# Performance work log

Measured on AMD Instinct MI355X. Metric: run time of the kernel, lower is better.

The kernel has to match this reference:

```python
import jax, jax.numpy as jnp
import numpy as np

T = 2048          # tokens (single causal sequence)
HID = 4096        # hidden_size
H = 32            # num_heads
DQ = 256          # per-head q/k dim (192 nope + 64 rope)
DN = 192          # nope dim
DR = 64           # rope dim
DV = 256          # v head dim
DKV = 512         # kv latent rank
QLORA = 2048      # q lora rank
EPS = 1e-6
THETA = 10000.0
SCALE = DQ ** -0.5


def rmsnorm(x, w):
    return x * jax.lax.rsqrt(jnp.mean(x * x, axis=-1, keepdims=True) + EPS) * w


def rope_neox(pos, x):
    # x: [T, h, DR]; neox style: rotate concatenated halves
    inv_freq = 1.0 / (THETA ** (jnp.arange(0, DR, 2, dtype=jnp.float32) / DR))  # [DR/2]
    ang = pos.astype(jnp.float32)[:, None] * inv_freq  # [T, DR/2]
    cos = jnp.cos(ang)[:, None, :]
    sin = jnp.sin(ang)[:, None, :]
    x1, x2 = jnp.split(x, 2, axis=-1)
    return jnp.concatenate([x1 * cos - x2 * sin, x2 * cos + x1 * sin], axis=-1)


def setup_inputs() -> dict:
    key = jax.random.key(0)
    ks = jax.random.split(key, 8)
    s = 0.02
    return {
        "hidden_states": jax.random.normal(ks[0], (T, HID), dtype=jnp.float32),
        "positions": jnp.arange(T, dtype=jnp.int32),
        "wq_a": jax.random.normal(ks[1], (HID, QLORA), dtype=jnp.float32) * s,
        "q_a_ln_w": jnp.ones((QLORA,), dtype=jnp.float32),
        "wq_b": jax.random.normal(ks[2], (QLORA, H * DQ), dtype=jnp.float32) * s,
        "wkv_a": jax.random.normal(ks[3], (HID, DKV + DR), dtype=jnp.float32) * s,
        "kv_a_ln_w": jnp.ones((DKV,), dtype=jnp.float32),
        "wkv_b": jax.random.normal(ks[4], (DKV, H * (DN + DV)), dtype=jnp.float32) * s,
        "wo": jax.random.normal(ks[5], (H * DV, HID), dtype=jnp.float32) * s,
    }


def reference(hidden_states, positions, wq_a, q_a_ln_w, wq_b, wkv_a, kv_a_ln_w, wkv_b, wo):
    # q path: lora down -> rmsnorm -> up -> [T, H, 256]
    q = rmsnorm(hidden_states @ wq_a, q_a_ln_w)
    q = (q @ wq_b).reshape(T, H, DQ)
    # kv path: latent 512 + shared k_pe 64
    latent = hidden_states @ wkv_a
    kv_a, k_pe = jnp.split(latent, [DKV], axis=-1)
    kv_a = rmsnorm(kv_a, kv_a_ln_w)
    kv = (kv_a @ wkv_b).reshape(T, H, DN + DV)
    k_nope, v = jnp.split(kv, [DN], axis=-1)
    q_nope, q_pe = jnp.split(q, [DN], axis=-1)
    k_pe = k_pe.reshape(T, 1, DR)
    q_pe = rope_neox(positions, q_pe)
    k_pe = rope_neox(positions, k_pe)
    q = jnp.concatenate([q_nope, q_pe], axis=-1)                       # [T, H, 256]
    k = jnp.concatenate([k_nope, jnp.broadcast_to(k_pe, (T, H, DR))], axis=-1)
    # causal attention
    scores = jnp.einsum("thd,shd->hts", q, k) * SCALE                  # [H, T, T]
    causal = jnp.tril(jnp.ones((T, T), dtype=bool))
    scores = jnp.where(causal[None], scores, jnp.finfo(scores.dtype).min)
    attn = jax.nn.softmax(scores, axis=-1)
    out = jnp.einsum("hts,shd->thd", attn, v).reshape(T, H * DV)
    return out @ wo
```

## Files before the change

kernel.cpp:

```cpp
#include <hip/hip_runtime.h>
#include <cstdint>
#include <cstddef>

#define T_    2048
#define HID_  4096
#define NH_   32
#define DQ_   256
#define DN_   192
#define DR_   64
#define DV_   256
#define DKV_  512
#define QL_   2048
#define NKV_  576
#define HDQ_  8192
#define HDKV_ 14336
#define HDV_  8192
#define SCALE_ 0.0625f
#define MN5_  8388608
#define SK5_  2
#define NKC_  2816
#define PS1_  5767168
#define SK1_  4

using bf16x8 = __attribute__((ext_vector_type(8))) short;
using f32x4  = __attribute__((ext_vector_type(4))) float;

__device__ ushort g_hb   [(size_t)T_*HID_];
__device__ ushort g_wtc  [(size_t)NKC_*HID_];
__device__ ushort g_wtqb [(size_t)HDQ_*QL_];
__device__ ushort g_wtkvb[(size_t)HDKV_*DKV_];
__device__ ushort g_wto  [(size_t)HID_*HDV_];
__device__ float  g_qa   [(size_t)T_*QL_];
__device__ ushort g_qn   [(size_t)T_*QL_];
__device__ ushort g_q    [(size_t)T_*HDQ_];
__device__ ushort g_kvn  [(size_t)T_*DKV_];
__device__ ushort g_kv   [(size_t)T_*HDKV_];
__device__ ushort g_k    [(size_t)NH_*T_*DQ_];
__device__ ushort g_vt   [(size_t)NH_*DV_*T_];
__device__ ushort g_o    [(size_t)T_*HDV_];
__device__ float  g_p5   [(size_t)SK1_*PS1_];

__device__ __forceinline__ float b2f(ushort h){ union{unsigned u; float f;} x; x.u=((unsigned)h)<<16; return x.f; }
__device__ __forceinline__ ushort f2b(float f){ union{float f; unsigned u;} x; x.f=f; unsigned r=x.u + 0x7fffu + ((x.u>>16)&1u); return (ushort)(r>>16); }
__device__ __forceinline__ void storeC(float*  p, float v){ *p = v; }
__device__ __forceinline__ void storeC(ushort* p, float v){ *p = f2b(v); }

#define GLD16(gp, lp) __builtin_amdgcn_global_load_lds( \
    (const __attribute__((address_space(1))) unsigned*)(gp), \
    (__attribute__((address_space(3))) unsigned*)(lp), 16, 0, 0)

__global__ __launch_bounds__(256) void convert_hidden(const float* __restrict__ src) {
  size_t i = ((size_t)blockIdx.x*256 + threadIdx.x)*4;
  float4 v = *(const float4*)(src + i);
  ushort4 o; o.x=f2b(v.x); o.y=f2b(v.y); o.z=f2b(v.z); o.w=f2b(v.w);
  *(ushort4*)(g_hb + i) = o;
}

__global__ __launch_bounds__(256) void transpose_all(const float* __restrict__ wqa,
                                                     const float* __restrict__ wkva,
                                                     const float* __restrict__ wqb,
                                                     const float* __restrict__ wkvb,
                                                     const float* __restrict__ wo) {
  int bid = blockIdx.x;
  const float* W; ushort* Wt; int K, N, gx;
  if (bid < 4096)       { W=wqa;  Wt=g_wtc;                      K=HID_; N=QL_;   gx=64; }
  else if (bid < 5632)  { W=wkva; Wt=g_wtc+(size_t)QL_*HID_;     K=HID_; N=NKV_;  gx=64;  bid-=4096; }
  else if (bid < 13824) { W=wqb;  Wt=g_wtqb;                     K=QL_;  N=HDQ_;  gx=32;  bid-=5632; }
  else if (bid < 17408) { W=wkvb; Wt=g_wtkvb;                    K=DKV_; N=HDKV_; gx=8;   bid-=13824; }
  else                  { W=wo;   Wt=g_wto;                      K=HDV_; N=HID_;  gx=128; bid-=17408; }
  const int bk = (bid % gx)*64, bn = (bid / gx)*32;

  __shared__ float tile[64][33];
  const int tx = threadIdx.x & 31, ty = threadIdx.x >> 5;
  for (int r = ty; r < 64; r += 8) {
    int n = bn + tx;
    tile[r][tx] = (n < N) ? W[(size_t)(bk + r)*N + n] : 0.f;
  }
  __syncthreads();
  for (int rr = ty; rr < 32; rr += 8) {
    int n = bn + rr;
    unsigned pv = (unsigned)f2b(tile[2*tx][rr]) | ((unsigned)f2b(tile[2*tx+1][rr]) << 16);
    ((unsigned*)(Wt + (size_t)n*K))[(bk>>1) + tx] = pv;
  }
}

template<typename OutT, int S, int EPI>
__device__ __forceinline__ void gemm8_body(ushort* sm,
                                           const ushort* __restrict__ A,
                                           const ushort* __restrict__ Bt,
                                           OutT* __restrict__ C,
                                           int M, int N, int Kfull, int pstride,
                                           int id, int nb) {
  const int tid = threadIdx.x, lane = tid & 63, w = tid >> 6;
  const int wr = w >> 2, wc = w & 3, l15 = lane & 15, l4 = lane >> 4;
  const int swm = (l15 & 7) << 3;
  const int gm = M >> 8, gn = N >> 8;
  const int swz = (id & 7) * (nb >> 3) + (id >> 3);
  const int m0 = (swz % gm) << 8;
  const int rest = swz / gm;
  const int n0 = (rest % gn) << 8;
  const int ks = rest / gn;
  const int Ksl = Kfull / S;
  const int kofs = ks * Ksl;
  const int NT = Ksl >> 6;

#define STG_A(tt, qm) do { const int p_=(tt)&1, kb_=kofs+(tt)*64; \
    _Pragma("unroll") \
    for (int i_=0;i_<2;i_++){ \
      const int le_=(i_*512+tid)*8, r_=le_>>6, c_=le_&63; \
      const int tr_=(r_>>6)*128 + (qm)*64 + (r_&63); \
      GLD16(A + (size_t)(m0+tr_)*Kfull + kb_ + (c_ ^ ((r_&7)<<3)), \
            sm + p_*16384 + (qm)*8192 + le_); } } while(0)
#define STG_B(tt, qn) do { const int p_=(tt)&1, kb_=kofs+(tt)*64; \
    _Pragma("unroll") \
    for (int i_=0;i_<2;i_++){ \
      const int le_=(i_*512+tid)*8, r_=le_>>6, c_=le_&63; \
      const int tr_=(r_>>5)*64 + (qn)*32 + (r_&31); \
      GLD16(Bt + (size_t)(n0+tr_)*Kfull + kb_ + (c_ ^ ((r_&7)<<3)), \
            sm + 32768 + p_*16384 + (qn)*8192 + le_); } } while(0)

  f32x4 acc[8][4];
  #pragma unroll
  for (int i=0;i<8;i++)
    #pragma unroll
    for (int j=0;j<4;j++) acc[i][j] = f32x4{0.f,0.f,0.f,0.f};

  STG_A(0,0); STG_B(0,0); STG_A(0,1); STG_B(0,1);
  if (NT > 1) { STG_A(1,0); STG_B(1,0); }
  __builtin_amdgcn_sched_barrier(0);
  if (NT > 1) asm volatile("s_waitcnt vmcnt(4)" ::: "memory");
  else        asm volatile("s_waitcnt vmcnt(0)" ::: "memory");
  __builtin_amdgcn_sched_barrier(0);
  __builtin_amdgcn_s_barrier();

  for (int t = 0; t < NT; ++t) {
    const int p = t & 1;
    const ushort* Ab = sm + p*16384;
    const ushort* Bb = sm + 32768 + p*16384;
    bf16x8 af[4][2], bq0[2][2], bq1[2][2];

    #pragma unroll
    for (int mi=0;mi<4;mi++)
      #pragma unroll
      for (int k2=0;k2<2;k2++)
        af[mi][k2] = *(const bf16x8*)(Ab + (wr*64 + mi*16 + l15)*64 + ((k2*32 + 8*l4) ^ swm));
    #pragma unroll
    for (int nf=0;nf<2;nf++)
      #pragma unroll
      for (int k2=0;k2<2;k2++)
        bq0[nf][k2] = *(const bf16x8*)(Bb + (wc*32 + nf*16 + l15)*64 + ((k2*32 + 8*l4) ^ swm));
    if (t + 1 < NT) STG_A(t+1, 1);
    __builtin_amdgcn_sched_barrier(0);
    __builtin_amdgcn_s_barrier();
    __builtin_amdgcn_s_setprio(1);
    #pragma unroll
    for (int mi=0;mi<4;mi++)
      #pragma unroll
      for (int nf=0;nf<2;nf++)
        #pragma unroll
        for (int k2=0;k2<2;k2++)
          acc[mi][nf] = __builtin_amdgcn_mfma_f32_16x16x32_bf16(af[mi][k2], bq0[nf][k2], acc[mi][nf], 0,0,0);
    __builtin_amdgcn_s_setprio(0);
    __builtin_amdgcn_sched_barrier(0);
    __builtin_amdgcn_s_barrier();

    #pragma unroll
    for (int nf=0;nf<2;nf++)
      #pragma unroll
      for (int k2=0;k2<2;k2++)
        bq1[nf][k2] = *(const bf16x8*)(Bb + 8192 + (wc*32 + nf*16 + l15)*64 + ((k2*32 + 8*l4) ^ swm));
    if (t + 1 < NT) STG_B(t+1, 1);
    __builtin_amdgcn_sched_barrier(0);
    __builtin_amdgcn_s_barrier();
    __builtin_amdgcn_s_setprio(1);
    #pragma unroll
    for (int mi=0;mi<4;mi++)
      #pragma unroll
      for (int nf=0;nf<2;nf++)
        #pragma unroll
        for (int k2=0;k2<2;k2++)
          acc[mi][2+nf] = __builtin_amdgcn_mfma_f32_16x16x32_bf16(af[mi][k2], bq1[nf][k2], acc[mi][2+nf], 0,0,0);
    __builtin_amdgcn_s_setprio(0);
    __builtin_amdgcn_sched_barrier(0);
    __builtin_amdgcn_s_barrier();

    #pragma unroll
    for (int mi=0;mi<4;mi++)
      #pragma unroll
      for (int k2=0;k2<2;k2++)
        af[mi][k2] = *(const bf16x8*)(Ab + 8192 + (wr*64 + mi*16 + l15)*64 + ((k2*32 + 8*l4) ^ swm));
    if (t + 2 < NT) STG_A(t+2, 0);
    __builtin_amdgcn_sched_barrier(0);
    __builtin_amdgcn_s_barrier();
    __builtin_amdgcn_s_setprio(1);
    #pragma unroll
    for (int mi=0;mi<4;mi++)
      #pragma unroll
      for (int nf=0;nf<2;nf++)
        #pragma unroll
        for (int k2=0;k2<2;k2++)
          acc[4+mi][nf] = __builtin_amdgcn_mfma_f32_16x16x32_bf16(af[mi][k2], bq0[nf][k2], acc[4+mi][nf], 0,0,0);
    __builtin_amdgcn_s_setprio(0);
    __builtin_amdgcn_sched_barrier(0);
    __builtin_amdgcn_s_barrier();

    if (t + 2 < NT) STG_B(t+2, 0);
    __builtin_amdgcn_sched_barrier(0);
    if (t + 2 < NT)      asm volatile("s_waitcnt vmcnt(4)" ::: "memory");
    else if (t + 1 < NT) asm volatile("s_waitcnt vmcnt(0)" ::: "memory");
    __builtin_amdgcn_sched_barrier(0);
    __builtin_amdgcn_s_barrier();
    __builtin_amdgcn_s_setprio(1);
    #pragma unroll
    for (int mi=0;mi<4;mi++)
      #pragma unroll
      for (int nf=0;nf<2;nf++)
        #pragma unroll
        for (int k2=0;k2<2;k2++)
          acc[4+mi][2+nf] = __builtin_amdgcn_mfma_f32_16x16x32_bf16(af[mi][k2], bq1[nf][k2], acc[4+mi][2+nf], 0,0,0);
    __builtin_amdgcn_s_setprio(0);
    __builtin_amdgcn_sched_barrier(0);
    __builtin_amdgcn_s_barrier();
  }
#undef STG_A
#undef STG_B
  asm volatile("s_waitcnt vmcnt(0)" ::: "memory");

  #pragma unroll
  for (int mi=0;mi<8;mi++)
    #pragma unroll
    for (int nj=0;nj<4;nj++) {
      const int row = m0 + wr*128 + mi*16 + l4*4;
      const int col = n0 + wc*64 + nj*16 + l15;
      if (EPI == 2) {
        const int h = col / 448, j = col - h*448;
        #pragma unroll
        for (int r=0;r<4;r++) {
          ushort v = f2b(acc[mi][nj][r]);
          if (j < DN_) g_k[((size_t)h*T_ + row + r)*DQ_ + j] = v;
          else         g_kv[(size_t)(row + r)*HDKV_ + col]   = v;
        }
      } else {
        #pragma unroll
        for (int r=0;r<4;r++) {
          if (S == 1) storeC(&C[(size_t)(row+r)*N + col], acc[mi][nj][r]);
          else ((float*)C)[(size_t)ks*pstride + (size_t)(row+r)*N + col] = acc[mi][nj][r];
        }
      }
    }
}

template<typename OutT, int S, int EPI>
__global__ __launch_bounds__(512, 2) void gemm8(const ushort* __restrict__ A,
                                                const ushort* __restrict__ Bt,
                                                OutT* __restrict__ C,
                                                int M, int N, int Kfull, int pstride) {
  __shared__ ushort sm[65536];
  gemm8_body<OutT,S,EPI>(sm, A, Bt, C, M, N, Kfull, pstride, blockIdx.x, gridDim.x);
}

__global__ __launch_bounds__(512, 2) void gemm_up_dual(const ushort* __restrict__ qn,
                                                       const ushort* __restrict__ wtqb,
                                                       ushort* __restrict__ q,
                                                       const ushort* __restrict__ kvn,
                                                       const ushort* __restrict__ wtkvb) {
  __shared__ ushort sm[65536];
  if (blockIdx.x < 256)
    gemm8_body<ushort,1,0>(sm, qn, wtqb, q, T_, HDQ_, QL_, 0, blockIdx.x, 256);
  else
    gemm8_body<ushort,1,2>(sm, kvn, wtkvb, (ushort*)nullptr, T_, HDKV_, DKV_, 0, blockIdx.x - 256, 448);
}

__global__ __launch_bounds__(256) void reduce5(const float* __restrict__ p, float* __restrict__ out) {
  size_t i = ((size_t)blockIdx.x*256 + threadIdx.x)*4;
  float4 a = *(const float4*)(p + i);
  #pragma unroll
  for (int s=1; s<SK5_; s++) {
    float4 b = *(const float4*)(p + (size_t)s*MN5_ + i);
    a.x+=b.x; a.y+=b.y; a.z+=b.z; a.w+=b.w;
  }
  *(float4*)(out + i) = a;
}

__global__ __launch_bounds__(256) void rmsnorm_q(const float* __restrict__ p,
                                                 const float* __restrict__ wln) {
  const int row = blockIdx.x;
  const float* x = p + (size_t)row*NKC_;
  float* xo = g_qa + (size_t)row*QL_;
  float ss = 0.f;
  for (int i = threadIdx.x; i < QL_/4; i += 256) {
    float4 v = *(const float4*)(x + i*4);
    #pragma unroll
    for (int s=1; s<SK1_; s++) {
      float4 b = *(const float4*)(x + (size_t)s*PS1_ + i*4);
      v.x+=b.x; v.y+=b.y; v.z+=b.z; v.w+=b.w;
    }
    ((float4*)xo)[i] = v;
    ss += v.x*v.x + v.y*v.y + v.z*v.z + v.w*v.w;
  }
  #pragma unroll
  for (int o=32;o>=1;o>>=1) ss += __shfl_xor(ss, o);
  __shared__ float sr[4];
  if ((threadIdx.x & 63) == 0) sr[threadIdx.x>>6] = ss;
  __syncthreads();
  float rs = rsqrtf((sr[0]+sr[1]+sr[2]+sr[3])/(float)QL_ + 1e-6f);
  for (int i = threadIdx.x; i < QL_; i += 256)
    g_qn[(size_t)row*QL_ + i] = f2b(xo[i]*rs*wln[i]);
}

__global__ __launch_bounds__(256) void kv_norm_rope(const float* __restrict__ p,
                                                    const float* __restrict__ wln,
                                                    const int* __restrict__ pos) {
  const int t = blockIdx.x;
  const float* base = p + (size_t)t*NKC_ + QL_;
  __shared__ float lat[NKV_];
  float ss = 0.f;
  for (int i = threadIdx.x; i < NKV_; i += 256) {
    float v = base[i];
    #pragma unroll
    for (int s=1; s<SK1_; s++) v += base[(size_t)s*PS1_ + i];
    lat[i] = v;
    if (i < DKV_) ss += v*v;
  }
  #pragma unroll
  for (int o=32;o>=1;o>>=1) ss += __shfl_xor(ss, o);
  __shared__ float sr[4];
  if ((threadIdx.x & 63) == 0) sr[threadIdx.x>>6] = ss;
  __syncthreads();
  float rs = rsqrtf((sr[0]+sr[1]+sr[2]+sr[3])/(float)DKV_ + 1e-6f);
  for (int i = threadIdx.x; i < DKV_; i += 256)
    g_kvn[(size_t)t*DKV_ + i] = f2b(lat[i]*rs*wln[i]);
  {
    const int i = threadIdx.x & 31, hb = threadIdx.x >> 5;
    float pp = (float)pos[t];
    float ang = pp * powf(10000.f, -(float)i/32.f);
    float c = cosf(ang), s = sinf(ang);
    float x1 = lat[DKV_ + i], x2 = lat[DKV_ + 32 + i];
    ushort k1 = f2b(x1*c - x2*s);
    ushort k2 = f2b(x2*c + x1*s);
    #pragma unroll
    for (int hh = 0; hh < 4; ++hh) {
      const int h = hb + hh*8;
      g_k[((size_t)h*T_ + t)*DQ_ + DN_ + i]      = k1;
      g_k[((size_t)h*T_ + t)*DQ_ + DN_ + 32 + i] = k2;
    }
  }
}

__global__ __launch_bounds__(256) void q_rope(const int* __restrict__ pos) {
  const int t = blockIdx.x;
  __shared__ float cs[32], sn[32];
  if (threadIdx.x < 32) {
    const int i = threadIdx.x;
    float p = (float)pos[t];
    float ang = p * powf(10000.f, -(float)i/32.f);
    cs[i] = cosf(ang); sn[i] = sinf(ang);
  }
  __syncthreads();
  for (int e = threadIdx.x; e < NH_*32; e += 256) {
    const int h = e >> 5, i = e & 31;
    ushort* qp = g_q + (size_t)t*HDQ_ + h*DQ_ + DN_;
    float x1 = b2f(qp[i]), x2 = b2f(qp[32 + i]);
    qp[i]      = f2b(x1*cs[i] - x2*sn[i]);
    qp[32 + i] = f2b(x2*cs[i] + x1*sn[i]);
  }
}

__global__ __launch_bounds__(256) void build_vt() {
  const int h = blockIdx.x, tt = blockIdx.y;
  __shared__ ushort tile[64*272];
  const int tid = threadIdx.x;
  #pragma unroll
  for (int p=0;p<8;p++) {
    int le = (p*256+tid)*8;
    int tl = le >> 8, d = le & 255;
    uint4 v = *(const uint4*)(g_kv + (size_t)(tt*64 + tl)*HDKV_ + h*448 + DN_ + d);
    *(uint4*)(tile + tl*272 + d) = v;
  }
  __syncthreads();
  #pragma unroll
  for (int p=0;p<8;p++) {
    int le = (p*256+tid)*8;
    int d = le >> 6, tl0 = le & 63;
    ushort tmp[8];
    #pragma unroll
    for (int j=0;j<8;j++) tmp[j] = tile[(tl0+j)*272 + d];
    *(uint4*)(g_vt + ((size_t)h*DV_ + d)*T_ + tt*64 + tl0) = *(const uint4*)tmp;
  }
}

__global__ __launch_bounds__(256) void attn_kernel() {
  __shared__ ushort KV[64*256];
  __shared__ ushort Pl[4][16][64];
  const int h = blockIdx.x;
  const int qt = (gridDim.y - 1) - blockIdx.y;
  const int tid = threadIdx.x, lane = tid & 63, w = tid >> 6;
  const int l15 = lane & 15, l4 = lane >> 4;
  const int swm = (l15 & 7) << 3;

  const ushort* Kh = g_k  + (size_t)h*T_*DQ_;
  const ushort* Vh = g_vt + (size_t)h*DV_*T_;

#define STAGE_K(kt_) do { \
    const ushort* ks_ = Kh + (size_t)(kt_)*64*DQ_; \
    _Pragma("unroll") \
    for (int c_=0;c_<8;c_++){ int le_=(c_*256+tid)*8, r_=le_>>8, co_=le_&255; \
      GLD16(ks_ + r_*256 + (co_ ^ ((r_&7)<<3)), KV+le_); } } while(0)
#define STAGE_V(kt_) do { \
    _Pragma("unroll") \
    for (int c_=0;c_<8;c_++){ int le_=(c_*256+tid)*8, d_=le_>>6, kv_=le_&63; \
      GLD16(Vh + (size_t)d_*T_ + (kt_)*64 + (kv_ ^ ((d_&7)<<3)), KV+le_); } } while(0)

  const int q0 = qt*64;
  const int qrow = q0 + w*16 + l15;

  bf16x8 qf[8];
  {
    const ushort* qb = g_q + (size_t)qrow*HDQ_ + h*DQ_;
    #pragma unroll
    for (int g=0; g<8; g++) qf[g] = *(const bf16x8*)(qb + 32*g + 8*l4);
  }
  f32x4 acc[16];
  #pragma unroll
  for (int i=0;i<16;i++) acc[i] = f32x4{0.f,0.f,0.f,0.f};
  float m_r = -1e30f, l_r = 0.f;

  STAGE_K(0);

  for (int kt = 0; kt <= qt; ++kt) {
    __builtin_amdgcn_sched_barrier(0);
    asm volatile("s_waitcnt vmcnt(0)" ::: "memory");
    __builtin_amdgcn_sched_barrier(0);
    __builtin_amdgcn_s_barrier();

    f32x4 s[4];
    #pragma unroll
    for (int fn=0; fn<4; fn++) s[fn] = f32x4{0.f,0.f,0.f,0.f};
    __builtin_amdgcn_s_setprio(1);
    #pragma unroll
    for (int g=0; g<8; g++)
      #pragma unroll
      for (int fn=0; fn<4; fn++) {
        bf16x8 kf = *(const bf16x8*)(KV + (fn*16 + l15)*256 + ((32*g + 8*l4) ^ swm));
        s[fn] = __builtin_amdgcn_mfma_f32_16x16x32_bf16(kf, qf[g], s[fn], 0,0,0);
      }
    __builtin_amdgcn_s_setprio(0);
    asm volatile("s_waitcnt lgkmcnt(0)" ::: "memory");
    __builtin_amdgcn_sched_barrier(0);
    __builtin_amdgcn_s_barrier();
    STAGE_V(kt);
    __builtin_amdgcn_sched_barrier(0);

    if (kt == qt) {
      #pragma unroll
      for (int fn=0; fn<4; fn++)
        #pragma unroll
        for (int r=0;r<4;r++) {
          int kv = kt*64 + fn*16 + l4*4 + r;
          if (kv > qrow) s[fn][r] = -1e30f;
        }
    }

    float mx = s[0][0];
    #pragma unroll
    for (int fn=0; fn<4; fn++)
      #pragma unroll
      for (int r=0;r<4;r++) mx = fmaxf(mx, s[fn][r]);
    mx = fmaxf(mx, __shfl_xor(mx, 16));
    mx = fmaxf(mx, __shfl_xor(mx, 32));
    mx *= SCALE_;
    if (__any(mx > m_r)) {
      float mn = fmaxf(m_r, mx);
      float sc = __expf(m_r - mn);
      m_r = mn;
      l_r *= sc;
      #pragma unroll
      for (int fd=0; fd<16; fd++)
        #pragma unroll
        for (int r=0;r<4;r++) acc[fd][r] *= sc;
    }
    float ssum = 0.f;
    #pragma unroll
    for (int fn=0; fn<4; fn++)
      #pragma unroll
      for (int r=0;r<4;r++) {
        float p = __expf(fmaf(s[fn][r], SCALE_, -m_r));
        s[fn][r] = p; ssum += p;
      }
    ssum += __shfl_xor(ssum, 16);
    ssum += __shfl_xor(ssum, 32);
    l_r += ssum;

    #pragma unroll
    for (int fn=0; fn<4; fn++) {
      ushort4 pw;
      pw.x = f2b(s[fn][0]); pw.y = f2b(s[fn][1]);
      pw.z = f2b(s[fn][2]); pw.w = f2b(s[fn][3]);
      *(ushort4*)(&Pl[w][l15][(fn*16 + l4*4) ^ swm]) = pw;
    }

    __builtin_amdgcn_sched_barrier(0);
    asm volatile("s_waitcnt vmcnt(0)" ::: "memory");
    __builtin_amdgcn_sched_barrier(0);
    __builtin_amdgcn_s_barrier();

    __builtin_amdgcn_s_setprio(1);
    #pragma unroll
    for (int s2=0; s2<2; s2++) {
      bf16x8 pa = *(const bf16x8*)(&Pl[w][l15][(s2*32 + 8*l4) ^ swm]);
      #pragma unroll
      for (int fd=0; fd<16; fd++) {
        bf16x8 vb = *(const bf16x8*)(KV + (fd*16 + l15)*64 + ((s2*32 + 8*l4) ^ swm));
        acc[fd] = __builtin_amdgcn_mfma_f32_16x16x32_bf16(vb, pa, acc[fd], 0,0,0);
      }
    }
    __builtin_amdgcn_s_setprio(0);
    asm volatile("s_waitcnt lgkmcnt(0)" ::: "memory");
    __builtin_amdgcn_sched_barrier(0);
    __builtin_amdgcn_s_barrier();
    if (kt < qt) STAGE_K(kt+1);
    __builtin_amdgcn_sched_barrier(0);
  }

  l_r = 1.f / l_r;
  #pragma unroll
  for (int fd=0; fd<16; fd++) {
    ushort4 ow;
    ow.x = f2b(acc[fd][0] * l_r); ow.y = f2b(acc[fd][1] * l_r);
    ow.z = f2b(acc[fd][2] * l_r); ow.w = f2b(acc[fd][3] * l_r);
    *(ushort4*)(g_o + (size_t)qrow*HDV_ + h*DV_ + fd*16 + l4*4) = ow;
  }
#undef STAGE_K
#undef STAGE_V
}

extern "C" void kernel_launch(void* const* d_in, const int* in_sizes, int n_in,
                              void* d_out, int out_size, void* d_ws, size_t ws_size,
                              hipStream_t stream) {
  (void)in_sizes; (void)n_in; (void)d_ws; (void)ws_size; (void)out_size;
  const float* hs    = (const float*)d_in[0];
  const int*   pos   = (const int*)  d_in[1];
  const float* wqa   = (const float*)d_in[2];
  const float* qlnw  = (const float*)d_in[3];
  const float* wqb   = (const float*)d_in[4];
  const float* wkva  = (const float*)d_in[5];
  const float* kvlnw = (const float*)d_in[6];
  const float* wkvb  = (const float*)d_in[7];
  const float* wo    = (const float*)d_in[8];
  float* out = (float*)d_out;

  void *p_hb, *p_wtc, *p_wtqb, *p_wtkvb, *p_wto;
  void *p_qn, *p_q, *p_kvn, *p_kv, *p_o, *p_p5;
  hipGetSymbolAddress(&p_hb,    HIP_SYMBOL(g_hb));
  hipGetSymbolAddress(&p_wtc,   HIP_SYMBOL(g_wtc));
  hipGetSymbolAddress(&p_wtqb,  HIP_SYMBOL(g_wtqb));
  hipGetSymbolAddress(&p_wtkvb, HIP_SYMBOL(g_wtkvb));
  hipGetSymbolAddress(&p_wto,   HIP_SYMBOL(g_wto));
  hipGetSymbolAddress(&p_qn,    HIP_SYMBOL(g_qn));
  hipGetSymbolAddress(&p_q,     HIP_SYMBOL(g_q));
  hipGetSymbolAddress(&p_kvn,   HIP_SYMBOL(g_kvn));
  hipGetSymbolAddress(&p_kv,    HIP_SYMBOL(g_kv));
  hipGetSymbolAddress(&p_o,     HIP_SYMBOL(g_o));
  hipGetSymbolAddress(&p_p5,    HIP_SYMBOL(g_p5));

  convert_hidden<<<8192, 256, 0, stream>>>(hs);
  transpose_all<<<33792, 256, 0, stream>>>(wqa, wkva, wqb, wkvb, wo);

  gemm8<float,SK1_,1><<<(T_/256)*(NKC_/256)*SK1_, 512, 0, stream>>>((const ushort*)p_hb, (const ushort*)p_wtc, (float*)p_p5, T_, NKC_, HID_, PS1_);
  rmsnorm_q<<<T_, 256, 0, stream>>>((const float*)p_p5, qlnw);
  kv_norm_rope<<<T_, 256, 0, stream>>>((const float*)p_p5, kvlnw, pos);

  gemm_up_dual<<<704, 512, 0, stream>>>((const ushort*)p_qn, (const ushort*)p_wtqb, (ushort*)p_q,
                                        (const ushort*)p_kvn, (const ushort*)p_wtkvb);
  q_rope<<<T_, 256, 0, stream>>>(pos);

  build_vt<<<dim3(NH_, T_/64), 256, 0, stream>>>();
  attn_kernel<<<dim3(NH_, 32), 256, 0, stream>>>();

  gemm8<float,SK5_,1><<<(T_/256)*(HID_/256)*SK5_, 512, 0, stream>>>((const ushort*)p_o, (const ushort*)p_wto, (float*)p_p5, T_, HID_, HDV_, MN5_);
  reduce5<<<MN5_/1024, 256, 0, stream>>>((const float*)p_p5, out);
}
```

Before: 747.1 us.

## Split K/V LDS buffers in attention and fold hidden conversion into transpose

The attention kernel now gives K and V^T their own shared-memory buffers, so both tiles are loaded together at the end of each iteration. This removes the mid-iteration wait and barrier pairs that existed only because the two tiles shared one buffer. The price is more LDS per block (about 72KB), which can lower how many blocks fit on a CU. Separately, the hidden-state fp32-to-bf16 conversion is folded into the weight transpose launch as extra blocks, saving one kernel launch.

Measured after the change: 759.8 us. Within noise of the previous version (+1.7%).

```diff
diff --git a/kernel.cpp b/kernel.cpp
--- a/kernel.cpp
+++ b/kernel.cpp
@@ -49,19 +49,21 @@
     (const __attribute__((address_space(1))) unsigned*)(gp), \
     (__attribute__((address_space(3))) unsigned*)(lp), 16, 0, 0)
 
-__global__ __launch_bounds__(256) void convert_hidden(const float* __restrict__ src) {
-  size_t i = ((size_t)blockIdx.x*256 + threadIdx.x)*4;
-  float4 v = *(const float4*)(src + i);
-  ushort4 o; o.x=f2b(v.x); o.y=f2b(v.y); o.z=f2b(v.z); o.w=f2b(v.w);
-  *(ushort4*)(g_hb + i) = o;
-}
-
-__global__ __launch_bounds__(256) void transpose_all(const float* __restrict__ wqa,
+__global__ __launch_bounds__(256) void transpose_all(const float* __restrict__ hs,
+                                                     const float* __restrict__ wqa,
                                                      const float* __restrict__ wkva,
                                                      const float* __restrict__ wqb,
                                                      const float* __restrict__ wkvb,
                                                      const float* __restrict__ wo) {
   int bid = blockIdx.x;
+  if (bid < 8192) {
+    size_t i = ((size_t)bid*256 + threadIdx.x)*4;
+    float4 v = *(const float4*)(hs + i);
+    ushort4 o; o.x=f2b(v.x); o.y=f2b(v.y); o.z=f2b(v.z); o.w=f2b(v.w);
+    *(ushort4*)(g_hb + i) = o;
+    return;
+  }
+  bid -= 8192;
   const float* W; ushort* Wt; int K, N, gx;
   if (bid < 4096)       { W=wqa;  Wt=g_wtc;                      K=HID_; N=QL_;   gx=64; }
   else if (bid < 5632)  { W=wkva; Wt=g_wtc+(size_t)QL_*HID_;     K=HID_; N=NKV_;  gx=64;  bid-=4096; }
@@ -390,7 +392,8 @@
 }
 
 __global__ __launch_bounds__(256) void attn_kernel() {
-  __shared__ ushort KV[64*256];
+  __shared__ ushort Ks [64*256];
+  __shared__ ushort Vts[256*64];
   __shared__ ushort Pl[4][16][64];
   const int h = blockIdx.x;
   const int qt = (gridDim.y - 1) - blockIdx.y;
@@ -405,11 +408,11 @@
     const ushort* ks_ = Kh + (size_t)(kt_)*64*DQ_; \
     _Pragma("unroll") \
     for (int c_=0;c_<8;c_++){ int le_=(c_*256+tid)*8, r_=le_>>8, co_=le_&255; \
-      GLD16(ks_ + r_*256 + (co_ ^ ((r_&7)<<3)), KV+le_); } } while(0)
+      GLD16(ks_ + r_*256 + (co_ ^ ((r_&7)<<3)), Ks+le_); } } while(0)
 #define STAGE_V(kt_) do { \
     _Pragma("unroll") \
     for (int c_=0;c_<8;c_++){ int le_=(c_*256+tid)*8, d_=le_>>6, kv_=le_&63; \
-      GLD16(Vh + (size_t)d_*T_ + (kt_)*64 + (kv_ ^ ((d_&7)<<3)), KV+le_); } } while(0)
+      GLD16(Vh + (size_t)d_*T_ + (kt_)*64 + (kv_ ^ ((d_&7)<<3)), Vts+le_); } } while(0)
 
   const int q0 = qt*64;
   const int qrow = q0 + w*16 + l15;
@@ -426,6 +429,7 @@
   float m_r = -1e30f, l_r = 0.f;
 
   STAGE_K(0);
+  STAGE_V(0);
 
   for (int kt = 0; kt <= qt; ++kt) {
     __builtin_amdgcn_sched_barrier(0);
@@ -441,15 +445,10 @@
     for (int g=0; g<8; g++)
       #pragma unroll
       for (int fn=0; fn<4; fn++) {
-        bf16x8 kf = *(const bf16x8*)(KV + (fn*16 + l15)*256 + ((32*g + 8*l4) ^ swm));
+        bf16x8 kf = *(const bf16x8*)(Ks + (fn*16 + l15)*256 + ((32*g + 8*l4) ^ swm));
         s[fn] = __builtin_amdgcn_mfma_f32_16x16x32_bf16(kf, qf[g], s[fn], 0,0,0);
       }
     __builtin_amdgcn_s_setprio(0);
-    asm volatile("s_waitcnt lgkmcnt(0)" ::: "memory");
-    __builtin_amdgcn_sched_barrier(0);
-    __builtin_amdgcn_s_barrier();
-    STAGE_V(kt);
-    __builtin_amdgcn_sched_barrier(0);
 
     if (kt == qt) {
       #pragma unroll
@@ -499,18 +498,13 @@
       *(ushort4*)(&Pl[w][l15][(fn*16 + l4*4) ^ swm]) = pw;
     }
 
-    __builtin_amdgcn_sched_barrier(0);
-    asm volatile("s_waitcnt vmcnt(0)" ::: "memory");
-    __builtin_amdgcn_sched_barrier(0);
-    __builtin_amdgcn_s_barrier();
-
     __builtin_amdgcn_s_setprio(1);
     #pragma unroll
     for (int s2=0; s2<2; s2++) {
       bf16x8 pa = *(const bf16x8*)(&Pl[w][l15][(s2*32 + 8*l4) ^ swm]);
       #pragma unroll
       for (int fd=0; fd<16; fd++) {
-        bf16x8 vb = *(const bf16x8*)(KV + (fd*16 + l15)*64 + ((s2*32 + 8*l4) ^ swm));
+        bf16x8 vb = *(const bf16x8*)(Vts + (fd*16 + l15)*64 + ((s2*32 + 8*l4) ^ swm));
         acc[fd] = __builtin_amdgcn_mfma_f32_16x16x32_bf16(vb, pa, acc[fd], 0,0,0);
       }
     }
@@ -518,7 +512,7 @@
     asm volatile("s_waitcnt lgkmcnt(0)" ::: "memory");
     __builtin_amdgcn_sched_barrier(0);
     __builtin_amdgcn_s_barrier();
-    if (kt < qt) STAGE_K(kt+1);
+    if (kt < qt) { STAGE_K(kt+1); STAGE_V(kt+1); }
     __builtin_amdgcn_sched_barrier(0);
   }
 
@@ -563,8 +557,7 @@
   hipGetSymbolAddress(&p_o,     HIP_SYMBOL(g_o));
   hipGetSymbolAddress(&p_p5,    HIP_SYMBOL(g_p5));
 
-  convert_hidden<<<8192, 256, 0, stream>>>(hs);
-  transpose_all<<<33792, 256, 0, stream>>>(wqa, wkva, wqb, wkvb, wo);
+  transpose_all<<<41984, 256, 0, stream>>>(hs, wqa, wkva, wqb, wkvb, wo);
 
   gemm8<float,SK1_,1><<<(T_/256)*(NKC_/256)*SK1_, 512, 0, stream>>>((const ushort*)p_hb, (const ushort*)p_wtc, (float*)p_p5, T_, NKC_, HID_, PS1_);
   rmsnorm_q<<<T_, 256, 0, stream>>>((const float*)p_p5, qlnw);
```
